# Performance work log

Hardware: AMD Instinct MI355X
Metric: run time of the kernel (lower is better)

Reference implementation:

```python
import jax, jax.numpy as jnp
import numpy as np

DIM = 2048
DIM_HEAD = 64
HEADS = 16
FF_MULT = 4
ATTN_INNER = DIM_HEAD * HEADS          # 1024
FF_INNER = DIM * FF_MULT               # 8192
FUSED = ATTN_INNER + DIM_HEAD + DIM_HEAD + FF_INNER  # 9344
EPS = 1e-8


def setup_inputs() -> dict:
    key = jax.random.key(0)
    ks = jax.random.split(key, 8)
    b, n = 2, 2048
    x = jax.random.normal(ks[0], (b, n, DIM), dtype=jnp.float32)
    g = jnp.ones((DIM,), dtype=jnp.float32)
    s = DIM ** -0.5
    W_fused = jax.random.normal(ks[1], (DIM, FUSED), dtype=jnp.float32) * s
    b_fused = jnp.zeros((FUSED,), dtype=jnp.float32)
    W_attn = jax.random.normal(ks[2], (ATTN_INNER, DIM), dtype=jnp.float32) * ATTN_INNER ** -0.5
    b_attn = jnp.zeros((DIM,), dtype=jnp.float32)
    W_ff = jax.random.normal(ks[3], (FF_INNER, DIM), dtype=jnp.float32) * FF_INNER ** -0.5
    b_ff = jnp.zeros((DIM,), dtype=jnp.float32)
    return {"x": x, "g": g, "W_fused": W_fused, "b_fused": b_fused,
            "W_attn": W_attn, "b_attn": b_attn, "W_ff": W_ff, "b_ff": b_ff}


def _rotate_half(t):
    # last dim split into 2 halves: (x1, x2) -> (-x2, x1)
    x1, x2 = jnp.split(t, 2, axis=-1)
    return jnp.concatenate((-x2, x1), axis=-1)


def _rotary_pos(n, dtype):
    inv_freq = 1.0 / (10000.0 ** (jnp.arange(0, DIM_HEAD, 2, dtype=dtype) / DIM_HEAD))
    freqs = jnp.arange(n, dtype=dtype)[:, None] * inv_freq[None, :]  # [n, d/2]
    return jnp.concatenate((freqs, freqs), axis=-1)                  # [n, d]


def reference(x, g, W_fused, b_fused, W_attn, b_attn, W_ff, b_ff):
    b, n, _ = x.shape
    # RMSNorm (torch-style: L2 norm scaled by dim^-0.5, clamped)
    norm = jnp.linalg.norm(x, axis=-1, keepdims=True) * (DIM ** -0.5)
    xn = x / jnp.maximum(norm, EPS) * g
    # fused qkv + ff projection
    proj = xn @ W_fused + b_fused
    q, k, v, ff = jnp.split(proj, [ATTN_INNER, ATTN_INNER + DIM_HEAD,
                                   ATTN_INNER + 2 * DIM_HEAD], axis=-1)
    q = q.reshape(b, n, HEADS, DIM_HEAD).transpose(0, 2, 1, 3)  # b h n d
    # rotary
    pos = _rotary_pos(n, x.dtype)                # [n, d]
    cos, sin = jnp.cos(pos), jnp.sin(pos)
    q = q * cos + _rotate_half(q) * sin          # broadcasts over b,h
    k = k * cos + _rotate_half(k) * sin          # [b, n, d]
    q = q * (DIM_HEAD ** -0.5)
    # multi-query attention
    sim = jnp.einsum('bhid,bjd->bhij', q, k)
    causal = jnp.triu(jnp.ones((n, n), dtype=bool), k=1)
    sim = jnp.where(causal, -jnp.finfo(sim.dtype).max, sim)
    attn = jax.nn.softmax(sim, axis=-1)
    out = jnp.einsum('bhij,bjd->bhid', attn, v)
    out = out.transpose(0, 2, 1, 3).reshape(b, n, ATTN_INNER)
    attn_out = out @ W_attn + b_attn
    ff_out = jax.nn.gelu(ff, approximate=False) @ W_ff + b_ff
    return attn_out + ff_out
```

## Files before the change

### kernel.cpp

```cpp
#include <hip/hip_runtime.h>
#include <cstdint>
#include <cstddef>

typedef __bf16 bf16_t;
using bf16x8 = __attribute__((ext_vector_type(8))) __bf16;
using f32x4  = __attribute__((ext_vector_type(4))) float;
using u16x4  = __attribute__((ext_vector_type(4))) unsigned short;

#define DEV __device__ __forceinline__

DEV void gload16(const void* g, void* l) {
  __builtin_amdgcn_global_load_lds((const __attribute__((address_space(1))) void*)g,
                                   (__attribute__((address_space(3))) void*)l, 16, 0, 0);
}

__global__ __launch_bounds__(256) void rope_table_kernel(float* cs) {
  int idx = blockIdx.x * 256 + threadIdx.x;
  if (idx >= 2048 * 64) return;
  int n = idx >> 6, d = idx & 63;
  int i = d & 31;
  float freq = (float)n * powf(10000.0f, -(float)i * (1.0f / 32.0f));
  cs[idx]          = cosf(freq);
  cs[131072 + idx] = sinf(freq);
}

__global__ __launch_bounds__(256) void transpose_cvt_kernel(
    const float* __restrict__ in, bf16_t* __restrict__ out,
    int R, int C, int ostride, int coff)
{
  __shared__ bf16_t T[64][80];
  const int c0 = blockIdx.x * 64, r0 = blockIdx.y * 64;
  const int t = threadIdx.x;
  const int lr = t >> 4;
  const int lc = (t & 15) * 4;
#pragma unroll
  for (int i = 0; i < 4; i++) {
    int r = lr + i * 16;
    float4 v = *(const float4*)(in + (size_t)(r0 + r) * C + c0 + lc);
    T[lc + 0][r] = (bf16_t)v.x;
    T[lc + 1][r] = (bf16_t)v.y;
    T[lc + 2][r] = (bf16_t)v.z;
    T[lc + 3][r] = (bf16_t)v.w;
  }
  __syncthreads();
  const int oc = t >> 2;
  const int rc = (t & 3) * 16;
  bf16_t* dst = out + (size_t)(c0 + oc) * ostride + coff + r0 + rc;
  *(bf16x8*)dst       = *(const bf16x8*)&T[oc][rc];
  *(bf16x8*)(dst + 8) = *(const bf16x8*)&T[oc][rc + 8];
}

__global__ __launch_bounds__(256) void rmsnorm_kernel(
    const float* __restrict__ x, const float* __restrict__ g, bf16_t* __restrict__ xn)
{
  const int rid = blockIdx.x;
  const int t = threadIdx.x;
  const float* xr = x + (size_t)rid * 2048;
  float4 v0 = *(const float4*)(xr + t * 8);
  float4 v1 = *(const float4*)(xr + t * 8 + 4);
  float ss = v0.x*v0.x + v0.y*v0.y + v0.z*v0.z + v0.w*v0.w
           + v1.x*v1.x + v1.y*v1.y + v1.z*v1.z + v1.w*v1.w;
#pragma unroll
  for (int m = 1; m < 64; m <<= 1) ss += __shfl_xor(ss, m);
  __shared__ float red[4];
  if ((t & 63) == 0) red[t >> 6] = ss;
  __syncthreads();
  float tot = red[0] + red[1] + red[2] + red[3];
  float norm = sqrtf(tot * (1.0f / 2048.0f));
  float inv = 1.0f / fmaxf(norm, 1e-8f);
  float4 g0 = *(const float4*)(g + t * 8);
  float4 g1 = *(const float4*)(g + t * 8 + 4);
  bf16x8 o;
  o[0] = (bf16_t)(v0.x * inv * g0.x);
  o[1] = (bf16_t)(v0.y * inv * g0.y);
  o[2] = (bf16_t)(v0.z * inv * g0.z);
  o[3] = (bf16_t)(v0.w * inv * g0.w);
  o[4] = (bf16_t)(v1.x * inv * g1.x);
  o[5] = (bf16_t)(v1.y * inv * g1.y);
  o[6] = (bf16_t)(v1.z * inv * g1.z);
  o[7] = (bf16_t)(v1.w * inv * g1.w);
  *(bf16x8*)(xn + (size_t)rid * 2048 + t * 8) = o;
}

__global__ __launch_bounds__(256) void qkv_rope_kernel(
    const bf16_t* __restrict__ qkv, const float* __restrict__ cs,
    bf16_t* __restrict__ qr, bf16_t* __restrict__ kr, bf16_t* __restrict__ vt)
{
  __shared__ float row[1152];
  const int rid = blockIdx.x;
  const int b = rid >> 11, n = rid & 2047;
  const bf16_t* src = qkv + (size_t)rid * 1152;
  for (int c = threadIdx.x; c < 1152; c += 256) row[c] = (float)src[c];
  __syncthreads();
  const float* cosr = cs + n * 64;
  const float* sinr = cs + 131072 + n * 64;
  for (int c = threadIdx.x; c < 1152; c += 256) {
    if (c < 1024) {
      int d = c & 63;
      float cv = cosr[d], sv = sinr[d];
      float x0 = row[c];
      float xr = (d < 32) ? -row[c + 32] : row[c - 32];
      int hh = c >> 6;
      qr[((size_t)(b * 16 + hh) * 2048 + n) * 64 + d] = (bf16_t)((x0 * cv + xr * sv) * 0.125f);
    } else if (c < 1088) {
      int d = c - 1024;
      float cv = cosr[d], sv = sinr[d];
      float x0 = row[c];
      float xr = (d < 32) ? -row[c + 32] : row[c - 32];
      kr[((size_t)b * 2048 + n) * 64 + d] = (bf16_t)(x0 * cv + xr * sv);
    } else {
      int d = c - 1088;
      vt[((size_t)b * 64 + d) * 2048 + n] = src[c];
    }
  }
}

template <int EPI>
__global__ __launch_bounds__(256, 2) void gemm_kernel(
    const bf16_t* __restrict__ A, const bf16_t* __restrict__ Bt, int K,
    const float* __restrict__ bias0, const float* __restrict__ bias1,
    bf16_t* __restrict__ out_qkv, bf16_t* __restrict__ out_ap,
    float* __restrict__ out_f)
{
  __shared__ bf16_t Ash[128 * 64];
  __shared__ bf16_t Bsh[128 * 64];
  const int tid = threadIdx.x;
  const int w = tid >> 6, lane = tid & 63;
  const int wr = w >> 1, wc = w & 1;
  const int nwg = gridDim.x;
  const int g2  = (blockIdx.x & 7) * (nwg >> 3) + (blockIdx.x >> 3);
  const int m0 = (g2 & 31) * 128, n0 = (g2 >> 5) * 128;
  const int l15 = lane & 15, g4 = lane >> 4;

  f32x4 acc[4][4];
#pragma unroll
  for (int i = 0; i < 4; i++)
#pragma unroll
    for (int j = 0; j < 4; j++) acc[i][j] = f32x4{0.f, 0.f, 0.f, 0.f};

  for (int ks = 0; ks < K; ks += 64) {
    __syncthreads();
#pragma unroll
    for (int i = 0; i < 4; i++) {
      int slot = w * 256 + i * 64 + lane;
      int row = slot >> 3, ch = slot & 7;
      int gch = ch ^ (row & 7);
      gload16(A + (size_t)(m0 + row) * K + ks + gch * 8, (char*)Ash + (w * 4 + i) * 1024);
    }
#pragma unroll
    for (int i = 0; i < 4; i++) {
      int slot = w * 256 + i * 64 + lane;
      int row = slot >> 3, ch = slot & 7;
      int gch = ch ^ (row & 7);
      gload16(Bt + (size_t)(n0 + row) * K + ks + gch * 8, (char*)Bsh + (w * 4 + i) * 1024);
    }
    __syncthreads();
    const char* Ab = (const char*)Ash;
    const char* Bb = (const char*)Bsh;
#pragma unroll
    for (int kc = 0; kc < 2; kc++) {
      bf16x8 af[4], bfr[4];
#pragma unroll
      for (int mi = 0; mi < 4; mi++) {
        int r = wr * 64 + mi * 16 + l15;
        af[mi] = *(const bf16x8*)(Ab + r * 128 + ((kc * 64 + g4 * 16) ^ ((r & 7) << 4)));
      }
#pragma unroll
      for (int ni = 0; ni < 4; ni++) {
        int r = wc * 64 + ni * 16 + l15;
        bfr[ni] = *(const bf16x8*)(Bb + r * 128 + ((kc * 64 + g4 * 16) ^ ((r & 7) << 4)));
      }
#pragma unroll
      for (int mi = 0; mi < 4; mi++)
#pragma unroll
        for (int ni = 0; ni < 4; ni++)
          acc[mi][ni] = __builtin_amdgcn_mfma_f32_16x16x32_bf16(af[mi], bfr[ni], acc[mi][ni], 0, 0, 0);
    }
  }

#pragma unroll
  for (int mi = 0; mi < 4; mi++) {
    const int rb = m0 + wr * 64 + mi * 16 + g4 * 4;
#pragma unroll
    for (int ni = 0; ni < 4; ni++) {
      const int c = n0 + wc * 64 + ni * 16 + l15;
      if (EPI == 0) {
        const float bz = bias0[c];
        if (n0 < 1152) {
#pragma unroll
          for (int j = 0; j < 4; j++)
            out_qkv[(size_t)(rb + j) * 1152 + c] = (bf16_t)(acc[mi][ni][j] + bz);
        } else {
#pragma unroll
          for (int j = 0; j < 4; j++) {
            float v = acc[mi][ni][j] + bz;
            float ge = 0.5f * v * (1.0f + erff(v * 0.70710678118f));
            out_ap[(size_t)(rb + j) * 9216 + (c - 128)] = (bf16_t)ge;
          }
        }
      } else {
        const float bz = bias0[c] + bias1[c];
#pragma unroll
        for (int j = 0; j < 4; j++)
          out_f[(size_t)(rb + j) * 2048 + c] = acc[mi][ni][j] + bz;
      }
    }
  }
}

__global__ __launch_bounds__(64) void attn_kernel(
    const bf16_t* __restrict__ qr, const bf16_t* __restrict__ kr,
    const bf16_t* __restrict__ vt, bf16_t* __restrict__ Ap)
{
  __shared__ bf16_t Ksh[64 * 64];
  __shared__ bf16_t Vsh[64 * 64];
  __shared__ bf16_t Psh[32 * 64];
  const int lane = threadIdx.x;
  const int l15 = lane & 15, g4 = lane >> 4;
  const int qt = blockIdx.x, bh = blockIdx.y;
  const int b = bh >> 4, h = bh & 15;
  const int q0 = qt * 32;

  bf16x8 bq[2][2];
  const bf16_t* qbase = qr + ((size_t)bh * 2048 + q0) * 64;
#pragma unroll
  for (int qi = 0; qi < 2; qi++)
#pragma unroll
    for (int kc = 0; kc < 2; kc++)
      bq[qi][kc] = *(const bf16x8*)(qbase + (qi * 16 + l15) * 64 + kc * 32 + g4 * 8);

  const bf16_t* kb = kr + (size_t)b * 2048 * 64;
  const bf16_t* vb = vt + (size_t)b * 64 * 2048;

  f32x4 acc_o[2][4];
#pragma unroll
  for (int i = 0; i < 2; i++)
#pragma unroll
    for (int j = 0; j < 4; j++) acc_o[i][j] = f32x4{0.f, 0.f, 0.f, 0.f};
  float m_run[2] = {-1e30f, -1e30f};
  float l_run[2] = {0.f, 0.f};
  const int tlast = (q0 + 31) >> 6;

  for (int t = 0; t <= tlast; ++t) {
    const int kv0 = t * 64;
#pragma unroll
    for (int i = 0; i < 8; i++) {
      int slot = i * 64 + lane;
      int row = slot >> 3, ch = slot & 7;
      int gch = ch ^ (row & 7);
      gload16(kb + (size_t)(kv0 + row) * 64 + gch * 8, (char*)Ksh + i * 1024);
    }
#pragma unroll
    for (int i = 0; i < 8; i++) {
      int slot = i * 64 + lane;
      int row = slot >> 3, ch = slot & 7;
      int gch = ch ^ (row & 7);
      gload16(vb + (size_t)row * 2048 + kv0 + gch * 8, (char*)Vsh + i * 1024);
    }
    __syncthreads();

    f32x4 st[4][2];
#pragma unroll
    for (int i = 0; i < 4; i++)
#pragma unroll
      for (int j = 0; j < 2; j++) st[i][j] = f32x4{0.f, 0.f, 0.f, 0.f};
    const char* Kb8 = (const char*)Ksh;
#pragma unroll
    for (int kc = 0; kc < 2; kc++) {
      bf16x8 ak[4];
#pragma unroll
      for (int ni = 0; ni < 4; ni++) {
        int r = ni * 16 + l15;
        ak[ni] = *(const bf16x8*)(Kb8 + r * 128 + ((kc * 64 + g4 * 16) ^ ((r & 7) << 4)));
      }
#pragma unroll
      for (int ni = 0; ni < 4; ni++)
#pragma unroll
        for (int qi = 0; qi < 2; qi++)
          st[ni][qi] = __builtin_amdgcn_mfma_f32_16x16x32_bf16(ak[ni], bq[qi][kc], st[ni][qi], 0, 0, 0);
    }

    if (t == tlast) {
#pragma unroll
      for (int ni = 0; ni < 4; ni++)
#pragma unroll
        for (int qi = 0; qi < 2; qi++)
#pragma unroll
          for (int j = 0; j < 4; j++) {
            int kv = kv0 + ni * 16 + g4 * 4 + j;
            int q  = q0 + qi * 16 + l15;
            if (kv > q) st[ni][qi][j] = -1e30f;
          }
    }

    float sc[2];
#pragma unroll
    for (int qi = 0; qi < 2; qi++) {
      float vm = -1e30f;
#pragma unroll
      for (int ni = 0; ni < 4; ni++)
#pragma unroll
        for (int j = 0; j < 4; j++) vm = fmaxf(vm, st[ni][qi][j]);
      vm = fmaxf(vm, __shfl_xor(vm, 16));
      vm = fmaxf(vm, __shfl_xor(vm, 32));
      float mn = fmaxf(m_run[qi], vm);
      sc[qi] = __expf(m_run[qi] - mn);
      float ps = 0.f;
#pragma unroll
      for (int ni = 0; ni < 4; ni++)
#pragma unroll
        for (int j = 0; j < 4; j++) {
          float p = __expf(st[ni][qi][j] - mn);
          st[ni][qi][j] = p;
          ps += p;
        }
      l_run[qi] = l_run[qi] * sc[qi] + ps;
      m_run[qi] = mn;
    }

#pragma unroll
    for (int mi = 0; mi < 2; mi++)
#pragma unroll
      for (int j = 0; j < 4; j++) {
        float f = __shfl(sc[mi], g4 * 4 + j);
#pragma unroll
        for (int nd = 0; nd < 4; nd++) acc_o[mi][nd][j] *= f;
      }

#pragma unroll
    for (int ni = 0; ni < 4; ni++)
#pragma unroll
      for (int qi = 0; qi < 2; qi++) {
        int q = qi * 16 + l15;
        int kv = ni * 16 + g4 * 4;
        u16x4 pw;
#pragma unroll
        for (int j = 0; j < 4; j++) {
          bf16_t pv = (bf16_t)st[ni][qi][j];
          pw[j] = __builtin_bit_cast(unsigned short, pv);
        }
        *(u16x4*)((char*)Psh + q * 128 + ((kv * 2) ^ ((q & 7) << 4))) = pw;
      }
    __syncthreads();

    const char* Pb8 = (const char*)Psh;
    const char* Vb8 = (const char*)Vsh;
#pragma unroll
    for (int kc = 0; kc < 2; kc++) {
      bf16x8 apf[2], bvf[4];
#pragma unroll
      for (int mi = 0; mi < 2; mi++) {
        int r = mi * 16 + l15;
        apf[mi] = *(const bf16x8*)(Pb8 + r * 128 + ((kc * 64 + g4 * 16) ^ ((r & 7) << 4)));
      }
#pragma unroll
      for (int nd = 0; nd < 4; nd++) {
        int r = nd * 16 + l15;
        bvf[nd] = *(const bf16x8*)(Vb8 + r * 128 + ((kc * 64 + g4 * 16) ^ ((r & 7) << 4)));
      }
#pragma unroll
      for (int mi = 0; mi < 2; mi++)
#pragma unroll
        for (int nd = 0; nd < 4; nd++)
          acc_o[mi][nd] = __builtin_amdgcn_mfma_f32_16x16x32_bf16(apf[mi], bvf[nd], acc_o[mi][nd], 0, 0, 0);
    }
    __syncthreads();
  }

#pragma unroll
  for (int qi = 0; qi < 2; qi++) {
    float l = l_run[qi];
    l += __shfl_xor(l, 16);
    l += __shfl_xor(l, 32);
    l_run[qi] = l;
  }
#pragma unroll
  for (int mi = 0; mi < 2; mi++)
#pragma unroll
    for (int j = 0; j < 4; j++) {
      float linv = 1.0f / __shfl(l_run[mi], g4 * 4 + j);
      int r = q0 + mi * 16 + g4 * 4 + j;
      bf16_t* orow = Ap + (size_t)(b * 2048 + r) * 9216 + h * 64;
#pragma unroll
      for (int nd = 0; nd < 4; nd++)
        orow[nd * 16 + l15] = (bf16_t)(acc_o[mi][nd][j] * linv);
    }
}

extern "C" void kernel_launch(void* const* d_in, const int* in_sizes, int n_in,
                              void* d_out, int out_size, void* d_ws, size_t ws_size,
                              hipStream_t stream)
{
  const float* x       = (const float*)d_in[0];
  const float* g       = (const float*)d_in[1];
  const float* W_fused = (const float*)d_in[2];
  const float* b_fused = (const float*)d_in[3];
  const float* W_attn  = (const float*)d_in[4];
  const float* b_attn  = (const float*)d_in[5];
  const float* W_ff    = (const float*)d_in[6];
  const float* b_ff    = (const float*)d_in[7];
  float* out = (float*)d_out;
  char* ws = (char*)d_ws;

  bf16_t* Wf_t = (bf16_t*)(ws + 0);
  bf16_t* xn   = (bf16_t*)(ws + 38273024);
  bf16_t* qkv  = (bf16_t*)(ws + 55050240);
  bf16_t* qr   = (bf16_t*)(ws + 64487424);
  bf16_t* kr   = (bf16_t*)(ws + 72876032);
  bf16_t* vt   = (bf16_t*)(ws + 73400320);
  float*  cs   = (float*)(ws + 73924608);
  bf16_t* Wc_t = (bf16_t*)(ws + 74973184);
  bf16_t* Ap   = (bf16_t*)(ws + 112721920);

  rope_table_kernel<<<512, 256, 0, stream>>>(cs);
  transpose_cvt_kernel<<<dim3(146, 32), 256, 0, stream>>>(W_fused, Wf_t, 2048, 9344, 2048, 0);
  transpose_cvt_kernel<<<dim3(32, 16),  256, 0, stream>>>(W_attn,  Wc_t, 1024, 2048, 9216, 0);
  transpose_cvt_kernel<<<dim3(32, 128), 256, 0, stream>>>(W_ff,    Wc_t, 8192, 2048, 9216, 1024);
  rmsnorm_kernel<<<4096, 256, 0, stream>>>(x, g, xn);
  gemm_kernel<0><<<2336, 256, 0, stream>>>(xn, Wf_t, 2048, b_fused, nullptr, qkv, Ap, nullptr);
  qkv_rope_kernel<<<4096, 256, 0, stream>>>(qkv, cs, qr, kr, vt);
  attn_kernel<<<dim3(64, 32), 64, 0, stream>>>(qr, kr, vt, Ap);
  gemm_kernel<1><<<512, 256, 0, stream>>>(Ap, Wc_t, 9216, b_attn, b_ff, nullptr, nullptr, out);
}
```

Before: 518.3 us.

## Fuse RoPE into QKV GEMM epilogue and share K/V tiles across four attention waves

The fused projection GEMM now applies bias, rotary embedding and the q scale in its epilogue. It writes q, k and transposed v directly, which removes the separate qkv_rope kernel and its intermediate buffer round-trip. The attention kernel now runs 4 waves per block over 128 query rows. They share one K/V tile in LDS and each wave keeps its own P buffer, which cuts redundant K/V global loads. The cost is causal imbalance across waves: waves past their last tile sit idle at barriers, and the rope epilogue adds scattered cos/sin table reads.

```diff
diff --git a/kernel.cpp b/kernel.cpp
--- a/kernel.cpp
+++ b/kernel.cpp
@@ -82,45 +82,13 @@
   *(bf16x8*)(xn + (size_t)rid * 2048 + t * 8) = o;
 }
 
-__global__ __launch_bounds__(256) void qkv_rope_kernel(
-    const bf16_t* __restrict__ qkv, const float* __restrict__ cs,
-    bf16_t* __restrict__ qr, bf16_t* __restrict__ kr, bf16_t* __restrict__ vt)
-{
-  __shared__ float row[1152];
-  const int rid = blockIdx.x;
-  const int b = rid >> 11, n = rid & 2047;
-  const bf16_t* src = qkv + (size_t)rid * 1152;
-  for (int c = threadIdx.x; c < 1152; c += 256) row[c] = (float)src[c];
-  __syncthreads();
-  const float* cosr = cs + n * 64;
-  const float* sinr = cs + 131072 + n * 64;
-  for (int c = threadIdx.x; c < 1152; c += 256) {
-    if (c < 1024) {
-      int d = c & 63;
-      float cv = cosr[d], sv = sinr[d];
-      float x0 = row[c];
-      float xr = (d < 32) ? -row[c + 32] : row[c - 32];
-      int hh = c >> 6;
-      qr[((size_t)(b * 16 + hh) * 2048 + n) * 64 + d] = (bf16_t)((x0 * cv + xr * sv) * 0.125f);
-    } else if (c < 1088) {
-      int d = c - 1024;
-      float cv = cosr[d], sv = sinr[d];
-      float x0 = row[c];
-      float xr = (d < 32) ? -row[c + 32] : row[c - 32];
-      kr[((size_t)b * 2048 + n) * 64 + d] = (bf16_t)(x0 * cv + xr * sv);
-    } else {
-      int d = c - 1088;
-      vt[((size_t)b * 64 + d) * 2048 + n] = src[c];
-    }
-  }
-}
-
 template <int EPI>
 __global__ __launch_bounds__(256, 2) void gemm_kernel(
     const bf16_t* __restrict__ A, const bf16_t* __restrict__ Bt, int K,
     const float* __restrict__ bias0, const float* __restrict__ bias1,
-    bf16_t* __restrict__ out_qkv, bf16_t* __restrict__ out_ap,
-    float* __restrict__ out_f)
+    const float* __restrict__ cs,
+    bf16_t* __restrict__ qr, bf16_t* __restrict__ kr, bf16_t* __restrict__ vt,
+    bf16_t* __restrict__ out_ap, float* __restrict__ out_f)
 {
   __shared__ bf16_t Ash[128 * 64];
   __shared__ bf16_t Bsh[128 * 64];
@@ -185,12 +153,40 @@
     for (int ni = 0; ni < 4; ni++) {
       const int c = n0 + wc * 64 + ni * 16 + l15;
       if (EPI == 0) {
-        const float bz = bias0[c];
-        if (n0 < 1152) {
-#pragma unroll
-          for (int j = 0; j < 4; j++)
-            out_qkv[(size_t)(rb + j) * 1152 + c] = (bf16_t)(acc[mi][ni][j] + bz);
+        if (n0 < 1024 || (n0 == 1024 && wc == 0)) {
+          const int d = ni * 16 + l15;
+          const float bz  = bias0[c];
+          const float bz2 = bias0[c ^ 32];
+#pragma unroll
+          for (int j = 0; j < 4; j++) {
+            const int r = rb + j;
+            const int n = r & 2047, bb = r >> 11;
+            float v0 = acc[mi][ni][j] + bz;
+            float vp = acc[mi][ni ^ 2][j] + bz2;
+            float rot = (ni < 2) ? -vp : vp;
+            float cv = cs[n * 64 + d];
+            float sv = cs[131072 + n * 64 + d];
+            float o = v0 * cv + rot * sv;
+            if (n0 < 1024) {
+              const int h = (n0 >> 6) + wc;
+              qr[((size_t)(bb * 16 + h) * 2048 + n) * 64 + d] = (bf16_t)(o * 0.125f);
+            } else {
+              kr[((size_t)bb * 2048 + n) * 64 + d] = (bf16_t)o;
+            }
+          }
+        } else if (n0 == 1024) {
+          const int d = ni * 16 + l15;
+          const float bz = bias0[c];
+          const int n4 = rb & 2047, bb = rb >> 11;
+          u16x4 pw;
+#pragma unroll
+          for (int j = 0; j < 4; j++) {
+            bf16_t pv = (bf16_t)(acc[mi][ni][j] + bz);
+            pw[j] = __builtin_bit_cast(unsigned short, pv);
+          }
+          *(u16x4*)(vt + ((size_t)bb * 64 + d) * 2048 + n4) = pw;
         } else {
+          const float bz = bias0[c];
 #pragma unroll
           for (int j = 0; j < 4; j++) {
             float v = acc[mi][ni][j] + bz;
@@ -208,21 +204,24 @@
   }
 }
 
-__global__ __launch_bounds__(64) void attn_kernel(
+__global__ __launch_bounds__(256) void attn_kernel(
     const bf16_t* __restrict__ qr, const bf16_t* __restrict__ kr,
     const bf16_t* __restrict__ vt, bf16_t* __restrict__ Ap)
 {
   __shared__ bf16_t Ksh[64 * 64];
   __shared__ bf16_t Vsh[64 * 64];
-  __shared__ bf16_t Psh[32 * 64];
-  const int lane = threadIdx.x;
+  __shared__ bf16_t Psh[4][32 * 64];
+  const int tid = threadIdx.x;
+  const int w = tid >> 6, lane = tid & 63;
   const int l15 = lane & 15, g4 = lane >> 4;
-  const int qt = blockIdx.x, bh = blockIdx.y;
+  const int wun = tid & ~63;
+  const int bh = blockIdx.y;
   const int b = bh >> 4, h = bh & 15;
-  const int q0 = qt * 32;
+  const int q0 = blockIdx.x * 128;
+  const int q0w = q0 + w * 32;
 
   bf16x8 bq[2][2];
-  const bf16_t* qbase = qr + ((size_t)bh * 2048 + q0) * 64;
+  const bf16_t* qbase = qr + ((size_t)bh * 2048 + q0w) * 64;
 #pragma unroll
   for (int qi = 0; qi < 2; qi++)
 #pragma unroll
@@ -239,130 +238,132 @@
     for (int j = 0; j < 4; j++) acc_o[i][j] = f32x4{0.f, 0.f, 0.f, 0.f};
   float m_run[2] = {-1e30f, -1e30f};
   float l_run[2] = {0.f, 0.f};
-  const int tlast = (q0 + 31) >> 6;
-
-  for (int t = 0; t <= tlast; ++t) {
+  const int btlast = (q0 + 127) >> 6;
+  const int wtlast = (q0w + 31) >> 6;
+
+  for (int t = 0; t <= btlast; ++t) {
     const int kv0 = t * 64;
 #pragma unroll
-    for (int i = 0; i < 8; i++) {
-      int slot = i * 64 + lane;
+    for (int i = 0; i < 2; i++) {
+      int slot = i * 256 + tid;
       int row = slot >> 3, ch = slot & 7;
       int gch = ch ^ (row & 7);
-      gload16(kb + (size_t)(kv0 + row) * 64 + gch * 8, (char*)Ksh + i * 1024);
-    }
-#pragma unroll
-    for (int i = 0; i < 8; i++) {
-      int slot = i * 64 + lane;
+      gload16(kb + (size_t)(kv0 + row) * 64 + gch * 8, (char*)Ksh + (i * 256 + wun) * 16);
+    }
+#pragma unroll
+    for (int i = 0; i < 2; i++) {
+      int slot = i * 256 + tid;
       int row = slot >> 3, ch = slot & 7;
       int gch = ch ^ (row & 7);
-      gload16(vb + (size_t)row * 2048 + kv0 + gch * 8, (char*)Vsh + i * 1024);
+      gload16(vb + (size_t)row * 2048 + kv0 + gch * 8, (char*)Vsh + (i * 256 + wun) * 16);
     }
     __syncthreads();
 
-    f32x4 st[4][2];
-#pragma unroll
-    for (int i = 0; i < 4; i++)
-#pragma unroll
-      for (int j = 0; j < 2; j++) st[i][j] = f32x4{0.f, 0.f, 0.f, 0.f};
-    const char* Kb8 = (const char*)Ksh;
-#pragma unroll
-    for (int kc = 0; kc < 2; kc++) {
-      bf16x8 ak[4];
-#pragma unroll
-      for (int ni = 0; ni < 4; ni++) {
-        int r = ni * 16 + l15;
-        ak[ni] = *(const bf16x8*)(Kb8 + r * 128 + ((kc * 64 + g4 * 16) ^ ((r & 7) << 4)));
-      }
+    if (t <= wtlast) {
+      f32x4 st[4][2];
+#pragma unroll
+      for (int i = 0; i < 4; i++)
+#pragma unroll
+        for (int j = 0; j < 2; j++) st[i][j] = f32x4{0.f, 0.f, 0.f, 0.f};
+      const char* Kb8 = (const char*)Ksh;
+#pragma unroll
+      for (int kc = 0; kc < 2; kc++) {
+        bf16x8 ak[4];
+#pragma unroll
+        for (int ni = 0; ni < 4; ni++) {
+          int r = ni * 16 + l15;
+          ak[ni] = *(const bf16x8*)(Kb8 + r * 128 + ((kc * 64 + g4 * 16) ^ ((r & 7) << 4)));
+        }
+#pragma unroll
+        for (int ni = 0; ni < 4; ni++)
+#pragma unroll
+          for (int qi = 0; qi < 2; qi++)
+            st[ni][qi] = __builtin_amdgcn_mfma_f32_16x16x32_bf16(ak[ni], bq[qi][kc], st[ni][qi], 0, 0, 0);
+      }
+
+      if (t == wtlast) {
+#pragma unroll
+        for (int ni = 0; ni < 4; ni++)
+#pragma unroll
+          for (int qi = 0; qi < 2; qi++)
+#pragma unroll
+            for (int j = 0; j < 4; j++) {
+              int kv = kv0 + ni * 16 + g4 * 4 + j;
+              int q  = q0w + qi * 16 + l15;
+              if (kv > q) st[ni][qi][j] = -1e30f;
+            }
+      }
+
+      float sc[2];
+#pragma unroll
+      for (int qi = 0; qi < 2; qi++) {
+        float vm = -1e30f;
+#pragma unroll
+        for (int ni = 0; ni < 4; ni++)
+#pragma unroll
+          for (int j = 0; j < 4; j++) vm = fmaxf(vm, st[ni][qi][j]);
+        vm = fmaxf(vm, __shfl_xor(vm, 16));
+        vm = fmaxf(vm, __shfl_xor(vm, 32));
+        float mn = fmaxf(m_run[qi], vm);
+        sc[qi] = __expf(m_run[qi] - mn);
+        float ps = 0.f;
+#pragma unroll
+        for (int ni = 0; ni < 4; ni++)
+#pragma unroll
+          for (int j = 0; j < 4; j++) {
+            float p = __expf(st[ni][qi][j] - mn);
+            st[ni][qi][j] = p;
+            ps += p;
+          }
+        l_run[qi] = l_run[qi] * sc[qi] + ps;
+        m_run[qi] = mn;
+      }
+
+#pragma unroll
+      for (int mi = 0; mi < 2; mi++)
+#pragma unroll
+        for (int j = 0; j < 4; j++) {
+          float f = __shfl(sc[mi], g4 * 4 + j);
+#pragma unroll
+          for (int nd = 0; nd < 4; nd++) acc_o[mi][nd][j] *= f;
+        }
+
 #pragma unroll
       for (int ni = 0; ni < 4; ni++)
 #pragma unroll
-        for (int qi = 0; qi < 2; qi++)
-          st[ni][qi] = __builtin_amdgcn_mfma_f32_16x16x32_bf16(ak[ni], bq[qi][kc], st[ni][qi], 0, 0, 0);
-    }
-
-    if (t == tlast) {
-#pragma unroll
-      for (int ni = 0; ni < 4; ni++)
-#pragma unroll
-        for (int qi = 0; qi < 2; qi++)
+        for (int qi = 0; qi < 2; qi++) {
+          int q = qi * 16 + l15;
+          int kv = ni * 16 + g4 * 4;
+          u16x4 pw;
 #pragma unroll
           for (int j = 0; j < 4; j++) {
-            int kv = kv0 + ni * 16 + g4 * 4 + j;
-            int q  = q0 + qi * 16 + l15;
-            if (kv > q) st[ni][qi][j] = -1e30f;
+            bf16_t pv = (bf16_t)st[ni][qi][j];
+            pw[j] = __builtin_bit_cast(unsigned short, pv);
           }
-    }
-
-    float sc[2];
-#pragma unroll
-    for (int qi = 0; qi < 2; qi++) {
-      float vm = -1e30f;
-#pragma unroll
-      for (int ni = 0; ni < 4; ni++)
-#pragma unroll
-        for (int j = 0; j < 4; j++) vm = fmaxf(vm, st[ni][qi][j]);
-      vm = fmaxf(vm, __shfl_xor(vm, 16));
-      vm = fmaxf(vm, __shfl_xor(vm, 32));
-      float mn = fmaxf(m_run[qi], vm);
-      sc[qi] = __expf(m_run[qi] - mn);
-      float ps = 0.f;
-#pragma unroll
-      for (int ni = 0; ni < 4; ni++)
-#pragma unroll
-        for (int j = 0; j < 4; j++) {
-          float p = __expf(st[ni][qi][j] - mn);
-          st[ni][qi][j] = p;
-          ps += p;
-        }
-      l_run[qi] = l_run[qi] * sc[qi] + ps;
-      m_run[qi] = mn;
-    }
-
-#pragma unroll
-    for (int mi = 0; mi < 2; mi++)
-#pragma unroll
-      for (int j = 0; j < 4; j++) {
-        float f = __shfl(sc[mi], g4 * 4 + j);
-#pragma unroll
-        for (int nd = 0; nd < 4; nd++) acc_o[mi][nd][j] *= f;
-      }
-
-#pragma unroll
-    for (int ni = 0; ni < 4; ni++)
-#pragma unroll
-      for (int qi = 0; qi < 2; qi++) {
-        int q = qi * 16 + l15;
-        int kv = ni * 16 + g4 * 4;
-        u16x4 pw;
-#pragma unroll
-        for (int j = 0; j < 4; j++) {
-          bf16_t pv = (bf16_t)st[ni][qi][j];
-          pw[j] = __builtin_bit_cast(unsigned short, pv);
-        }
-        *(u16x4*)((char*)Psh + q * 128 + ((kv * 2) ^ ((q & 7) << 4))) = pw;
-      }
-    __syncthreads();
-
-    const char* Pb8 = (const char*)Psh;
-    const char* Vb8 = (const char*)Vsh;
-#pragma unroll
-    for (int kc = 0; kc < 2; kc++) {
-      bf16x8 apf[2], bvf[4];
-#pragma unroll
-      for (int mi = 0; mi < 2; mi++) {
-        int r = mi * 16 + l15;
-        apf[mi] = *(const bf16x8*)(Pb8 + r * 128 + ((kc * 64 + g4 * 16) ^ ((r & 7) << 4)));
-      }
-#pragma unroll
-      for (int nd = 0; nd < 4; nd++) {
-        int r = nd * 16 + l15;
-        bvf[nd] = *(const bf16x8*)(Vb8 + r * 128 + ((kc * 64 + g4 * 16) ^ ((r & 7) << 4)));
-      }
-#pragma unroll
-      for (int mi = 0; mi < 2; mi++)
-#pragma unroll
-        for (int nd = 0; nd < 4; nd++)
-          acc_o[mi][nd] = __builtin_amdgcn_mfma_f32_16x16x32_bf16(apf[mi], bvf[nd], acc_o[mi][nd], 0, 0, 0);
+          *(u16x4*)((char*)Psh[w] + q * 128 + ((kv * 2) ^ ((q & 7) << 4))) = pw;
+        }
+
+      const char* Pb8 = (const char*)Psh[w];
+      const char* Vb8 = (const char*)Vsh;
+#pragma unroll
+      for (int kc = 0; kc < 2; kc++) {
+        bf16x8 apf[2], bvf[4];
+#pragma unroll
+        for (int mi = 0; mi < 2; mi++) {
+          int r = mi * 16 + l15;
+          apf[mi] = *(const bf16x8*)(Pb8 + r * 128 + ((kc * 64 + g4 * 16) ^ ((r & 7) << 4)));
+        }
+#pragma unroll
+        for (int nd = 0; nd < 4; nd++) {
+          int r = nd * 16 + l15;
+          bvf[nd] = *(const bf16x8*)(Vb8 + r * 128 + ((kc * 64 + g4 * 16) ^ ((r & 7) << 4)));
+        }
+#pragma unroll
+        for (int mi = 0; mi < 2; mi++)
+#pragma unroll
+          for (int nd = 0; nd < 4; nd++)
+            acc_o[mi][nd] = __builtin_amdgcn_mfma_f32_16x16x32_bf16(apf[mi], bvf[nd], acc_o[mi][nd], 0, 0, 0);
+      }
     }
     __syncthreads();
   }
@@ -379,7 +380,7 @@
 #pragma unroll
     for (int j = 0; j < 4; j++) {
       float linv = 1.0f / __shfl(l_run[mi], g4 * 4 + j);
-      int r = q0 + mi * 16 + g4 * 4 + j;
+      int r = q0w + mi * 16 + g4 * 4 + j;
       bf16_t* orow = Ap + (size_t)(b * 2048 + r) * 9216 + h * 64;
 #pragma unroll
       for (int nd = 0; nd < 4; nd++)
@@ -404,21 +405,21 @@
 
   bf16_t* Wf_t = (bf16_t*)(ws + 0);
   bf16_t* xn   = (bf16_t*)(ws + 38273024);
-  bf16_t* qkv  = (bf16_t*)(ws + 55050240);
-  bf16_t* qr   = (bf16_t*)(ws + 64487424);
-  bf16_t* kr   = (bf16_t*)(ws + 72876032);
-  bf16_t* vt   = (bf16_t*)(ws + 73400320);
-  float*  cs   = (float*)(ws + 73924608);
-  bf16_t* Wc_t = (bf16_t*)(ws + 74973184);
-  bf16_t* Ap   = (bf16_t*)(ws + 112721920);
+  bf16_t* qr   = (bf16_t*)(ws + 55050240);
+  bf16_t* kr   = (bf16_t*)(ws + 63438848);
+  bf16_t* vt   = (bf16_t*)(ws + 63963136);
+  float*  cs   = (float*)(ws + 64487424);
+  bf16_t* Wc_t = (bf16_t*)(ws + 65536000);
+  bf16_t* Ap   = (bf16_t*)(ws + 103284736);
 
   rope_table_kernel<<<512, 256, 0, stream>>>(cs);
   transpose_cvt_kernel<<<dim3(146, 32), 256, 0, stream>>>(W_fused, Wf_t, 2048, 9344, 2048, 0);
   transpose_cvt_kernel<<<dim3(32, 16),  256, 0, stream>>>(W_attn,  Wc_t, 1024, 2048, 9216, 0);
   transpose_cvt_kernel<<<dim3(32, 128), 256, 0, stream>>>(W_ff,    Wc_t, 8192, 2048, 9216, 1024);
   rmsnorm_kernel<<<4096, 256, 0, stream>>>(x, g, xn);
-  gemm_kernel<0><<<2336, 256, 0, stream>>>(xn, Wf_t, 2048, b_fused, nullptr, qkv, Ap, nullptr);
-  qkv_rope_kernel<<<4096, 256, 0, stream>>>(qkv, cs, qr, kr, vt);
-  attn_kernel<<<dim3(64, 32), 64, 0, stream>>>(qr, kr, vt, Ap);
-  gemm_kernel<1><<<512, 256, 0, stream>>>(Ap, Wc_t, 9216, b_attn, b_ff, nullptr, nullptr, out);
-}
+  gemm_kernel<0><<<2336, 256, 0, stream>>>(xn, Wf_t, 2048, b_fused, nullptr, cs,
+                                           qr, kr, vt, Ap, nullptr);
+  attn_kernel<<<dim3(16, 32), 256, 0, stream>>>(qr, kr, vt, Ap);
+  gemm_kernel<1><<<512, 256, 0, stream>>>(Ap, Wc_t, 9216, b_attn, b_ff, nullptr,
+                                          nullptr, nullptr, nullptr, nullptr, out);
+}
```

Result: faster. 504.3 us (-2.7%).
